# Optimization experiments

Measured on AMD Instinct MI355X. Metric: run time of the kernel, lower is better.

The kernel has to match this reference:

```python
import jax, jax.numpy as jnp
import numpy as np

B, S, V, D, C = 2048, 256, 30522, 768, 100


def setup_inputs() -> dict:
    key = jax.random.key(0)
    k_ids, k_mask, k_emb, k_w1, k_b1, k_w2, k_b2 = jax.random.split(key, 7)
    input_ids = jax.random.randint(k_ids, (B, S), 0, V, dtype=jnp.int64)
    # ensure at least one valid token per row (avoid 0/0 in masked mean)
    attention_mask = jax.random.randint(k_mask, (B, S), 0, 2, dtype=jnp.int64)
    attention_mask = attention_mask.at[:, 0].set(1)
    scale = 1.0 / np.sqrt(D)
    return {
        "input_ids": input_ids,
        "attention_mask": attention_mask,
        "embed_table": jax.random.normal(k_emb, (V, D), dtype=jnp.float32) * 0.02,
        "W1": jax.random.normal(k_w1, (D, D), dtype=jnp.float32) * scale,
        "b1": jax.random.normal(k_b1, (D,), dtype=jnp.float32) * 0.01,
        "W2": jax.random.normal(k_w2, (D, C), dtype=jnp.float32) * scale,
        "b2": jax.random.normal(k_b2, (C,), dtype=jnp.float32) * 0.01,
    }


def reference(input_ids, attention_mask, embed_table, W1, b1, W2, b2):
    # Embedding lookup: [B, S, D]
    word_features = embed_table[input_ids]
    # Fused masked mean pooling over the whole batch (replaces python loop):
    # sum of valid token embeddings / count of valid tokens, per sample.
    mask = attention_mask.astype(word_features.dtype)          # [B, S]
    summed = jnp.einsum("bsd,bs->bd", word_features, mask)     # [B, D]
    counts = jnp.sum(mask, axis=1, keepdims=True)              # [B, 1]
    bow_features = summed / counts                              # [B, D]
    # 2-layer MLP head
    h = jax.nn.relu(bow_features @ W1 + b1)                     # [B, D]
    target_scores = h @ W2 + b2                                 # [B, C]
    return (target_scores, target_scores)
```

## Files before the change

kernel.cpp:

```cpp
#include <hip/hip_runtime.h>

#define B_ 2048
#define S_ 256
#define V_ 30522
#define D_ 768
#define C_ 100
#define NPAD 112

__device__ __forceinline__ unsigned short f2bf(float x) {
  unsigned u = __builtin_bit_cast(unsigned, x);
  u = (u + 0x7fffu + ((u >> 16) & 1u)) >> 16;
  return (unsigned short)u;
}

typedef __attribute__((ext_vector_type(8))) short bf16x8;
typedef __attribute__((ext_vector_type(4))) float f32x4;

__global__ __launch_bounds__(256) void prep_kernel(
    const int* __restrict__ ids, const int* __restrict__ mask,
    const float* __restrict__ w1, const float* __restrict__ w2,
    int* __restrict__ cids, int* __restrict__ cnts,
    unsigned short* __restrict__ w1t, unsigned short* __restrict__ w2t) {
  const int bid = blockIdx.x;
  if (bid < 512) {
    const int wv = threadIdx.x >> 6, lane = threadIdx.x & 63;
    const int b = bid * 4 + wv;
    const int base = b * S_;
    int total = 0;
#pragma unroll
    for (int r = 0; r < S_ / 64; ++r) {
      const int s = r * 64 + lane;
      const int m = mask[base + s];
      const unsigned long long bal = __ballot(m != 0);
      const int pre = __popcll(bal & ((1ull << lane) - 1ull));
      if (m) cids[base + total + pre] = ids[base + s];
      total += __popcll(bal);
    }
    if (lane == 0) cnts[b] = total;
  } else if (bid < 1088) {
    __shared__ float tile[32][33];
    const int local = bid - 512;
    const int k0 = (local % 24) * 32, n0 = (local / 24) * 32;
    const int tx = threadIdx.x & 31, ty = threadIdx.x >> 5;
#pragma unroll
    for (int i = 0; i < 4; ++i)
      tile[ty + i * 8][tx] = w1[(size_t)(k0 + ty + i * 8) * D_ + n0 + tx];
    __syncthreads();
#pragma unroll
    for (int i = 0; i < 4; ++i) {
      const int n = ty + i * 8;
      w1t[(size_t)(n0 + n) * D_ + k0 + tx] = f2bf(tile[tx][n]);
    }
  } else {
    __shared__ float tile[32][33];
    const int local = bid - 1088;
    const int k0 = (local % 24) * 32, n0 = (local / 24) * 32;
    const int tx = threadIdx.x & 31, ty = threadIdx.x >> 5;
#pragma unroll
    for (int i = 0; i < 4; ++i) {
      const int k = k0 + ty + i * 8, n = n0 + tx;
      tile[ty + i * 8][tx] = (n < C_) ? w2[(size_t)k * C_ + n] : 0.f;
    }
    __syncthreads();
#pragma unroll
    for (int i = 0; i < 4; ++i) {
      const int n = n0 + ty + i * 8;
      if (n < NPAD)
        w2t[(size_t)n * D_ + k0 + tx] = f2bf(tile[tx][ty + i * 8]);
    }
  }
}

__global__ __launch_bounds__(256) void pool_sliced(
    const int* __restrict__ cids, const int* __restrict__ cnts,
    const float* __restrict__ table, unsigned short* __restrict__ bowb,
    int pass) {
  __shared__ int sids[4][S_];
  const int bid = blockIdx.x;
  const int chunk = pass * 8 + (bid & 7);
  const int grp = bid >> 3;
  const int wv = threadIdx.x >> 6;
  const int lane = threadIdx.x & 63;
  const int sub = lane >> 3;
  const int cg = lane & 7;
  const int coff = chunk * 32 + cg * 4;

  for (int i = 0; i < 2; ++i) {
    const int smp = grp * 8 + wv * 2 + i;
    const int cnt = cnts[smp];
    const int* cp = cids + (size_t)smp * S_;
#pragma unroll
    for (int r = 0; r < S_ / 64; ++r) {
      const int idx = r * 64 + lane;
      sids[wv][idx] = (idx < cnt) ? cp[idx] : cp[0];
    }
    float a0 = 0.f, a1 = 0.f, a2 = 0.f, a3 = 0.f;
    for (int base = 0; base < cnt; base += 64) {
      float4 v[8];
#pragma unroll
      for (int j = 0; j < 8; ++j) {
        int t = base + j * 8 + sub;
        t = t < S_ ? t : S_ - 1;
        const int id = sids[wv][t];
        v[j] = *reinterpret_cast<const float4*>(table + (size_t)id * D_ + coff);
      }
#pragma unroll
      for (int j = 0; j < 8; ++j) {
        if (base + j * 8 + sub < cnt) {
          a0 += v[j].x; a1 += v[j].y; a2 += v[j].z; a3 += v[j].w;
        }
      }
    }
#pragma unroll
    for (int m = 8; m <= 32; m <<= 1) {
      a0 += __shfl_xor(a0, m);
      a1 += __shfl_xor(a1, m);
      a2 += __shfl_xor(a2, m);
      a3 += __shfl_xor(a3, m);
    }
    if (sub == 0) {
      const float inv = 1.0f / (float)cnt;
      ushort4 o;
      o.x = f2bf(a0 * inv); o.y = f2bf(a1 * inv);
      o.z = f2bf(a2 * inv); o.w = f2bf(a3 * inv);
      *reinterpret_cast<ushort4*>(bowb + (size_t)smp * D_ + coff) = o;
    }
  }
}

#define G1_BM 32
#define G1_BN 64
#define G1_LDK 72

__global__ __launch_bounds__(256) void gemm1_mfma(
    const unsigned short* __restrict__ Ab, const unsigned short* __restrict__ Bt,
    const float* __restrict__ bias, unsigned short* __restrict__ Hb) {
  __shared__ unsigned short As[G1_BM][G1_LDK];
  __shared__ unsigned short Bs[G1_BN][G1_LDK];
  const int tid = threadIdx.x;
  const int bm = blockIdx.x * G1_BM;
  const int bn = blockIdx.y * G1_BN;
  const int w = tid >> 6;
  const int l = tid & 63;
  const int r = l & 15;
  const int g = l >> 4;

  f32x4 acc0 = {0.f, 0.f, 0.f, 0.f};
  f32x4 acc1 = {0.f, 0.f, 0.f, 0.f};

  const int ar = tid >> 3;
  const int kc8 = (tid & 7) * 8;
  const int br = tid >> 3;

  for (int k0 = 0; k0 < D_; k0 += 64) {
    __syncthreads();
    *reinterpret_cast<int4*>(&As[ar][kc8]) =
        *reinterpret_cast<const int4*>(&Ab[(size_t)(bm + ar) * D_ + k0 + kc8]);
    *reinterpret_cast<int4*>(&Bs[br][kc8]) =
        *reinterpret_cast<const int4*>(&Bt[(size_t)(bn + br) * D_ + k0 + kc8]);
    *reinterpret_cast<int4*>(&Bs[br + 32][kc8]) =
        *reinterpret_cast<const int4*>(&Bt[(size_t)(bn + br + 32) * D_ + k0 + kc8]);
    __syncthreads();
    const bf16x8 a00 = *reinterpret_cast<const bf16x8*>(&As[r][g * 8]);
    const bf16x8 a01 = *reinterpret_cast<const bf16x8*>(&As[r][32 + g * 8]);
    const bf16x8 a10 = *reinterpret_cast<const bf16x8*>(&As[16 + r][g * 8]);
    const bf16x8 a11 = *reinterpret_cast<const bf16x8*>(&As[16 + r][32 + g * 8]);
    const bf16x8 b0 = *reinterpret_cast<const bf16x8*>(&Bs[w * 16 + r][g * 8]);
    const bf16x8 b1 = *reinterpret_cast<const bf16x8*>(&Bs[w * 16 + r][32 + g * 8]);
    acc0 = __builtin_amdgcn_mfma_f32_16x16x32_bf16(a00, b0, acc0, 0, 0, 0);
    acc0 = __builtin_amdgcn_mfma_f32_16x16x32_bf16(a01, b1, acc0, 0, 0, 0);
    acc1 = __builtin_amdgcn_mfma_f32_16x16x32_bf16(a10, b0, acc1, 0, 0, 0);
    acc1 = __builtin_amdgcn_mfma_f32_16x16x32_bf16(a11, b1, acc1, 0, 0, 0);
  }

  const int col = bn + w * 16 + r;
  const float bb = bias[col];
#pragma unroll
  for (int q = 0; q < 4; ++q) {
    const int row0 = bm + g * 4 + q;
    float v0 = acc0[q] + bb;
    v0 = v0 > 0.f ? v0 : 0.f;
    Hb[(size_t)row0 * D_ + col] = f2bf(v0);
    float v1 = acc1[q] + bb;
    v1 = v1 > 0.f ? v1 : 0.f;
    Hb[(size_t)(row0 + 16) * D_ + col] = f2bf(v1);
  }
}

__global__ __launch_bounds__(64) void gemm2_mfma(
    const unsigned short* __restrict__ Hb, const unsigned short* __restrict__ w2t,
    const float* __restrict__ b2, float* __restrict__ out) {
  const int bm = blockIdx.x * 16;
  const int bn = blockIdx.y * 16;
  const int l = threadIdx.x;
  const int r = l & 15;
  const int g = l >> 4;

  const unsigned short* ap = Hb + (size_t)(bm + r) * D_ + g * 8;
  const unsigned short* bp = w2t + (size_t)(bn + r) * D_ + g * 8;

  f32x4 acc = {0.f, 0.f, 0.f, 0.f};
#pragma unroll
  for (int k0 = 0; k0 < D_; k0 += 32) {
    const bf16x8 av = *reinterpret_cast<const bf16x8*>(ap + k0);
    const bf16x8 bv = *reinterpret_cast<const bf16x8*>(bp + k0);
    acc = __builtin_amdgcn_mfma_f32_16x16x32_bf16(av, bv, acc, 0, 0, 0);
  }

  const int col = bn + r;
  if (col < C_) {
    const float bb = b2[col];
#pragma unroll
    for (int q = 0; q < 4; ++q) {
      const int row = bm + g * 4 + q;
      const float v = acc[q] + bb;
      out[(size_t)row * C_ + col] = v;
      out[(size_t)row * C_ + col + (size_t)B_ * C_] = v;
    }
  }
}

extern "C" void kernel_launch(void* const* d_in, const int* in_sizes, int n_in,
                              void* d_out, int out_size, void* d_ws,
                              size_t ws_size, hipStream_t stream) {
  const int* ids = (const int*)d_in[0];
  const int* mask = (const int*)d_in[1];
  const float* table = (const float*)d_in[2];
  const float* W1 = (const float*)d_in[3];
  const float* b1 = (const float*)d_in[4];
  const float* W2 = (const float*)d_in[5];
  const float* b2 = (const float*)d_in[6];
  float* out = (float*)d_out;

  const size_t BOWB = (size_t)B_ * D_ * 2;
  const size_t HBB  = (size_t)B_ * D_ * 2;
  const size_t W1TB = (size_t)D_ * D_ * 2;
  const size_t W2TB = (size_t)NPAD * D_ * 2;
  const size_t CIDB = (size_t)B_ * S_ * 4;

  char* p = (char*)d_ws;
  unsigned short* bowb = (unsigned short*)p;
  unsigned short* hb   = (unsigned short*)(p + BOWB);
  unsigned short* w1t  = (unsigned short*)(p + BOWB + HBB);
  unsigned short* w2t  = (unsigned short*)(p + BOWB + HBB + W1TB);
  int* cids            = (int*)(p + BOWB + HBB + W1TB + W2TB);
  int* cnts            = (int*)(p + BOWB + HBB + W1TB + W2TB + CIDB);

  prep_kernel<<<1184, 256, 0, stream>>>(ids, mask, W1, W2, cids, cnts, w1t, w2t);
  pool_sliced<<<2048, 256, 0, stream>>>(cids, cnts, table, bowb, 0);
  pool_sliced<<<2048, 256, 0, stream>>>(cids, cnts, table, bowb, 1);
  pool_sliced<<<2048, 256, 0, stream>>>(cids, cnts, table, bowb, 2);
  gemm1_mfma<<<dim3(B_ / G1_BM, D_ / G1_BN), 256, 0, stream>>>(bowb, w1t, b1, hb);
  gemm2_mfma<<<dim3(B_ / 16, NPAD / 16), 64, 0, stream>>>(hb, w2t, b2, out);
}
```

Baseline: 95.53 us.

## Pin pooling column slices to XCCs via hardware ID and atomic work queue

The pooling kernel now reads the hardware XCC id and uses it to pick which 32-column slice of the embedding table a block handles, so each XCC's L2 only holds its own slice. Blocks take sample groups from a per-slice atomic counter, and the first blocks warm that XCC's L2 by touching a range of table rows. Counters are zeroed in an extra prep block. The aim is fewer L2 misses and less cross-die traffic during the random gathers, at the cost of atomics, extra syncs and a warm-up read.

```diff
diff --git a/kernel.cpp b/kernel.cpp
--- a/kernel.cpp
+++ b/kernel.cpp
@@ -7,6 +7,8 @@
 #define C_ 100
 #define NPAD 112
 
+#define XCC_ID_IMM 6164
+
 __device__ __forceinline__ unsigned short f2bf(float x) {
   unsigned u = __builtin_bit_cast(unsigned, x);
   u = (u + 0x7fffu + ((u >> 16) & 1u)) >> 16;
@@ -20,7 +22,8 @@
     const int* __restrict__ ids, const int* __restrict__ mask,
     const float* __restrict__ w1, const float* __restrict__ w2,
     int* __restrict__ cids, int* __restrict__ cnts,
-    unsigned short* __restrict__ w1t, unsigned short* __restrict__ w2t) {
+    unsigned short* __restrict__ w1t, unsigned short* __restrict__ w2t,
+    int* __restrict__ ctrs) {
   const int bid = blockIdx.x;
   if (bid < 512) {
     const int wv = threadIdx.x >> 6, lane = threadIdx.x & 63;
@@ -51,7 +54,7 @@
       const int n = ty + i * 8;
       w1t[(size_t)(n0 + n) * D_ + k0 + tx] = f2bf(tile[tx][n]);
     }
-  } else {
+  } else if (bid < 1184) {
     __shared__ float tile[32][33];
     const int local = bid - 1088;
     const int k0 = (local % 24) * 32, n0 = (local / 24) * 32;
@@ -68,63 +71,92 @@
       if (n < NPAD)
         w2t[(size_t)n * D_ + k0 + tx] = f2bf(tile[tx][ty + i * 8]);
     }
-  }
-}
+  } else {
+    if (threadIdx.x < 32) ctrs[threadIdx.x] = 0;
+  }
+}
+
+#define NGRP 256
+#define WARM_ROWS 120
 
 __global__ __launch_bounds__(256) void pool_sliced(
     const int* __restrict__ cids, const int* __restrict__ cnts,
     const float* __restrict__ table, unsigned short* __restrict__ bowb,
-    int pass) {
+    int* __restrict__ ctrs, int pass) {
   __shared__ int sids[4][S_];
-  const int bid = blockIdx.x;
-  const int chunk = pass * 8 + (bid & 7);
-  const int grp = bid >> 3;
-  const int wv = threadIdx.x >> 6;
-  const int lane = threadIdx.x & 63;
+  __shared__ int s_grp;
+  const int tid = threadIdx.x;
+  const int xcc = __builtin_amdgcn_s_getreg(XCC_ID_IMM) & 7;
+  const int chunk = pass * 8 + xcc;
+  const int coff0 = chunk * 32;
+
+  const int wv = tid >> 6;
+  const int lane = tid & 63;
   const int sub = lane >> 3;
   const int cg = lane & 7;
-  const int coff = chunk * 32 + cg * 4;
-
-  for (int i = 0; i < 2; ++i) {
-    const int smp = grp * 8 + wv * 2 + i;
-    const int cnt = cnts[smp];
-    const int* cp = cids + (size_t)smp * S_;
-#pragma unroll
-    for (int r = 0; r < S_ / 64; ++r) {
-      const int idx = r * 64 + lane;
-      sids[wv][idx] = (idx < cnt) ? cp[idx] : cp[0];
-    }
-    float a0 = 0.f, a1 = 0.f, a2 = 0.f, a3 = 0.f;
-    for (int base = 0; base < cnt; base += 64) {
-      float4 v[8];
-#pragma unroll
-      for (int j = 0; j < 8; ++j) {
-        int t = base + j * 8 + sub;
-        t = t < S_ ? t : S_ - 1;
-        const int id = sids[wv][t];
-        v[j] = *reinterpret_cast<const float4*>(table + (size_t)id * D_ + coff);
-      }
-#pragma unroll
-      for (int j = 0; j < 8; ++j) {
-        if (base + j * 8 + sub < cnt) {
-          a0 += v[j].x; a1 += v[j].y; a2 += v[j].z; a3 += v[j].w;
+  const int coff = coff0 + cg * 4;
+
+  if (tid == 0) s_grp = atomicAdd(&ctrs[chunk], 1);
+  __syncthreads();
+  int grp = s_grp;
+
+  if (grp < NGRP) {
+    const int r0 = grp * WARM_ROWS;
+    const int nr = (V_ - r0) < WARM_ROWS ? (V_ - r0) : WARM_ROWS;
+    float dummy = 0.f;
+    for (int i = tid; i < nr * 32; i += 256) {
+      const int row = r0 + (i >> 5);
+      dummy += table[(size_t)row * D_ + coff0 + (i & 31)];
+    }
+    asm volatile("" :: "v"(dummy));
+  }
+
+  while (grp < NGRP) {
+    for (int i = 0; i < 2; ++i) {
+      const int smp = grp * 8 + wv * 2 + i;
+      const int cnt = cnts[smp];
+      const int* cp = cids + (size_t)smp * S_;
+#pragma unroll
+      for (int r = 0; r < S_ / 64; ++r) {
+        const int idx = r * 64 + lane;
+        sids[wv][idx] = (idx < cnt) ? cp[idx] : cp[0];
+      }
+      float a0 = 0.f, a1 = 0.f, a2 = 0.f, a3 = 0.f;
+      for (int base = 0; base < cnt; base += 64) {
+        float4 v[8];
+#pragma unroll
+        for (int j = 0; j < 8; ++j) {
+          int t = base + j * 8 + sub;
+          t = t < S_ ? t : S_ - 1;
+          const int id = sids[wv][t];
+          v[j] = *reinterpret_cast<const float4*>(table + (size_t)id * D_ + coff);
         }
-      }
-    }
-#pragma unroll
-    for (int m = 8; m <= 32; m <<= 1) {
-      a0 += __shfl_xor(a0, m);
-      a1 += __shfl_xor(a1, m);
-      a2 += __shfl_xor(a2, m);
-      a3 += __shfl_xor(a3, m);
-    }
-    if (sub == 0) {
-      const float inv = 1.0f / (float)cnt;
-      ushort4 o;
-      o.x = f2bf(a0 * inv); o.y = f2bf(a1 * inv);
-      o.z = f2bf(a2 * inv); o.w = f2bf(a3 * inv);
-      *reinterpret_cast<ushort4*>(bowb + (size_t)smp * D_ + coff) = o;
-    }
+#pragma unroll
+        for (int j = 0; j < 8; ++j) {
+          if (base + j * 8 + sub < cnt) {
+            a0 += v[j].x; a1 += v[j].y; a2 += v[j].z; a3 += v[j].w;
+          }
+        }
+      }
+#pragma unroll
+      for (int m = 8; m <= 32; m <<= 1) {
+        a0 += __shfl_xor(a0, m);
+        a1 += __shfl_xor(a1, m);
+        a2 += __shfl_xor(a2, m);
+        a3 += __shfl_xor(a3, m);
+      }
+      if (sub == 0) {
+        const float inv = 1.0f / (float)cnt;
+        ushort4 o;
+        o.x = f2bf(a0 * inv); o.y = f2bf(a1 * inv);
+        o.z = f2bf(a2 * inv); o.w = f2bf(a3 * inv);
+        *reinterpret_cast<ushort4*>(bowb + (size_t)smp * D_ + coff) = o;
+      }
+    }
+    __syncthreads();
+    if (tid == 0) s_grp = atomicAdd(&ctrs[chunk], 1);
+    __syncthreads();
+    grp = s_grp;
   }
 }
 
@@ -150,16 +182,15 @@
 
   const int ar = tid >> 3;
   const int kc8 = (tid & 7) * 8;
-  const int br = tid >> 3;
 
   for (int k0 = 0; k0 < D_; k0 += 64) {
     __syncthreads();
     *reinterpret_cast<int4*>(&As[ar][kc8]) =
         *reinterpret_cast<const int4*>(&Ab[(size_t)(bm + ar) * D_ + k0 + kc8]);
-    *reinterpret_cast<int4*>(&Bs[br][kc8]) =
-        *reinterpret_cast<const int4*>(&Bt[(size_t)(bn + br) * D_ + k0 + kc8]);
-    *reinterpret_cast<int4*>(&Bs[br + 32][kc8]) =
-        *reinterpret_cast<const int4*>(&Bt[(size_t)(bn + br + 32) * D_ + k0 + kc8]);
+    *reinterpret_cast<int4*>(&Bs[ar][kc8]) =
+        *reinterpret_cast<const int4*>(&Bt[(size_t)(bn + ar) * D_ + k0 + kc8]);
+    *reinterpret_cast<int4*>(&Bs[ar + 32][kc8]) =
+        *reinterpret_cast<const int4*>(&Bt[(size_t)(bn + ar + 32) * D_ + k0 + kc8]);
     __syncthreads();
     const bf16x8 a00 = *reinterpret_cast<const bf16x8*>(&As[r][g * 8]);
     const bf16x8 a01 = *reinterpret_cast<const bf16x8*>(&As[r][32 + g * 8]);
@@ -237,6 +268,7 @@
   const size_t W1TB = (size_t)D_ * D_ * 2;
   const size_t W2TB = (size_t)NPAD * D_ * 2;
   const size_t CIDB = (size_t)B_ * S_ * 4;
+  const size_t CNTB = (size_t)B_ * 4;
 
   char* p = (char*)d_ws;
   unsigned short* bowb = (unsigned short*)p;
@@ -245,11 +277,13 @@
   unsigned short* w2t  = (unsigned short*)(p + BOWB + HBB + W1TB);
   int* cids            = (int*)(p + BOWB + HBB + W1TB + W2TB);
   int* cnts            = (int*)(p + BOWB + HBB + W1TB + W2TB + CIDB);
-
-  prep_kernel<<<1184, 256, 0, stream>>>(ids, mask, W1, W2, cids, cnts, w1t, w2t);
-  pool_sliced<<<2048, 256, 0, stream>>>(cids, cnts, table, bowb, 0);
-  pool_sliced<<<2048, 256, 0, stream>>>(cids, cnts, table, bowb, 1);
-  pool_sliced<<<2048, 256, 0, stream>>>(cids, cnts, table, bowb, 2);
+  int* ctrs            = (int*)(p + BOWB + HBB + W1TB + W2TB + CIDB + CNTB);
+
+  prep_kernel<<<1185, 256, 0, stream>>>(ids, mask, W1, W2, cids, cnts, w1t,
+                                        w2t, ctrs);
+  pool_sliced<<<2048, 256, 0, stream>>>(cids, cnts, table, bowb, ctrs, 0);
+  pool_sliced<<<2048, 256, 0, stream>>>(cids, cnts, table, bowb, ctrs, 1);
+  pool_sliced<<<2048, 256, 0, stream>>>(cids, cnts, table, bowb, ctrs, 2);
   gemm1_mfma<<<dim3(B_ / G1_BM, D_ / G1_BN), 256, 0, stream>>>(bowb, w1t, b1, hb);
   gemm2_mfma<<<dim3(B_ / 16, NPAD / 16), 64, 0, stream>>>(hb, w2t, b2, out);
 }
```

New measurement: 202.5 us. +111.9%, slower.

## Fuse three pooling passes into one kernel and drop per-token masking

Applied to the files above, without the earlier changes.

Merges the three pool_sliced launches into a single launch that loops over the three column passes internally, cutting launch overhead and inter-kernel gaps. The inner accumulation drops the per-token bounds check and clamp: padded slots are filled with the first valid id, summed unconditionally, and then corrected by subtracting the padding count times that row. This shortens the inner loop, but each block now does three times the work serially, and the padding correction can introduce small floating-point differences. The remaining edits rename variables in prep_kernel and gemm1 and do not change behavior.

```diff
diff --git a/kernel.cpp b/kernel.cpp
--- a/kernel.cpp
+++ b/kernel.cpp
@@ -22,8 +22,9 @@
     int* __restrict__ cids, int* __restrict__ cnts,
     unsigned short* __restrict__ w1t, unsigned short* __restrict__ w2t) {
   const int bid = blockIdx.x;
+  const int t = threadIdx.x;
   if (bid < 512) {
-    const int wv = threadIdx.x >> 6, lane = threadIdx.x & 63;
+    const int wv = t >> 6, lane = t & 63;
     const int b = bid * 4 + wv;
     const int base = b * S_;
     int total = 0;
@@ -41,7 +42,7 @@
     __shared__ float tile[32][33];
     const int local = bid - 512;
     const int k0 = (local % 24) * 32, n0 = (local / 24) * 32;
-    const int tx = threadIdx.x & 31, ty = threadIdx.x >> 5;
+    const int tx = t & 31, ty = t >> 5;
 #pragma unroll
     for (int i = 0; i < 4; ++i)
       tile[ty + i * 8][tx] = w1[(size_t)(k0 + ty + i * 8) * D_ + n0 + tx];
@@ -55,7 +56,7 @@
     __shared__ float tile[32][33];
     const int local = bid - 1088;
     const int k0 = (local % 24) * 32, n0 = (local / 24) * 32;
-    const int tx = threadIdx.x & 31, ty = threadIdx.x >> 5;
+    const int tx = t & 31, ty = t >> 5;
 #pragma unroll
     for (int i = 0; i < 4; ++i) {
       const int k = k0 + ty + i * 8, n = n0 + tx;
@@ -73,57 +74,60 @@
 
 __global__ __launch_bounds__(256) void pool_sliced(
     const int* __restrict__ cids, const int* __restrict__ cnts,
-    const float* __restrict__ table, unsigned short* __restrict__ bowb,
-    int pass) {
+    const float* __restrict__ table, unsigned short* __restrict__ bowb) {
   __shared__ int sids[4][S_];
   const int bid = blockIdx.x;
-  const int chunk = pass * 8 + (bid & 7);
   const int grp = bid >> 3;
   const int wv = threadIdx.x >> 6;
   const int lane = threadIdx.x & 63;
   const int sub = lane >> 3;
   const int cg = lane & 7;
-  const int coff = chunk * 32 + cg * 4;
-
-  for (int i = 0; i < 2; ++i) {
-    const int smp = grp * 8 + wv * 2 + i;
-    const int cnt = cnts[smp];
-    const int* cp = cids + (size_t)smp * S_;
-#pragma unroll
-    for (int r = 0; r < S_ / 64; ++r) {
-      const int idx = r * 64 + lane;
-      sids[wv][idx] = (idx < cnt) ? cp[idx] : cp[0];
-    }
-    float a0 = 0.f, a1 = 0.f, a2 = 0.f, a3 = 0.f;
-    for (int base = 0; base < cnt; base += 64) {
-      float4 v[8];
-#pragma unroll
-      for (int j = 0; j < 8; ++j) {
-        int t = base + j * 8 + sub;
-        t = t < S_ ? t : S_ - 1;
-        const int id = sids[wv][t];
-        v[j] = *reinterpret_cast<const float4*>(table + (size_t)id * D_ + coff);
-      }
-#pragma unroll
-      for (int j = 0; j < 8; ++j) {
-        if (base + j * 8 + sub < cnt) {
+
+  for (int pass = 0; pass < 3; ++pass) {
+    const int chunk = pass * 8 + (bid & 7);
+    const int coff = chunk * 32 + cg * 4;
+    for (int i = 0; i < 2; ++i) {
+      const int smp = grp * 8 + wv * 2 + i;
+      const int cnt = cnts[smp];
+      const int* cp = cids + (size_t)smp * S_;
+      const int id0 = cp[0];
+#pragma unroll
+      for (int r = 0; r < S_ / 64; ++r) {
+        const int idx = r * 64 + lane;
+        sids[wv][idx] = (idx < cnt) ? cp[idx] : id0;
+      }
+      float a0 = 0.f, a1 = 0.f, a2 = 0.f, a3 = 0.f;
+      const int nb = (cnt + 63) >> 6;
+      for (int b = 0; b < nb; ++b) {
+        float4 v[8];
+#pragma unroll
+        for (int j = 0; j < 8; ++j) {
+          const int id = sids[wv][b * 64 + j * 8 + sub];
+          v[j] = *reinterpret_cast<const float4*>(table + (size_t)id * D_ + coff);
+        }
+#pragma unroll
+        for (int j = 0; j < 8; ++j) {
           a0 += v[j].x; a1 += v[j].y; a2 += v[j].z; a3 += v[j].w;
         }
       }
-    }
-#pragma unroll
-    for (int m = 8; m <= 32; m <<= 1) {
-      a0 += __shfl_xor(a0, m);
-      a1 += __shfl_xor(a1, m);
-      a2 += __shfl_xor(a2, m);
-      a3 += __shfl_xor(a3, m);
-    }
-    if (sub == 0) {
-      const float inv = 1.0f / (float)cnt;
-      ushort4 o;
-      o.x = f2bf(a0 * inv); o.y = f2bf(a1 * inv);
-      o.z = f2bf(a2 * inv); o.w = f2bf(a3 * inv);
-      *reinterpret_cast<ushort4*>(bowb + (size_t)smp * D_ + coff) = o;
+#pragma unroll
+      for (int m = 8; m <= 32; m <<= 1) {
+        a0 += __shfl_xor(a0, m);
+        a1 += __shfl_xor(a1, m);
+        a2 += __shfl_xor(a2, m);
+        a3 += __shfl_xor(a3, m);
+      }
+      if (sub == 0) {
+        const float fp = (float)(nb * 64 - cnt);
+        const float4 v0 =
+            *reinterpret_cast<const float4*>(table + (size_t)id0 * D_ + coff);
+        a0 -= fp * v0.x; a1 -= fp * v0.y; a2 -= fp * v0.z; a3 -= fp * v0.w;
+        const float inv = 1.0f / (float)cnt;
+        ushort4 o;
+        o.x = f2bf(a0 * inv); o.y = f2bf(a1 * inv);
+        o.z = f2bf(a2 * inv); o.w = f2bf(a3 * inv);
+        *reinterpret_cast<ushort4*>(bowb + (size_t)smp * D_ + coff) = o;
+      }
     }
   }
 }
@@ -150,16 +154,15 @@
 
   const int ar = tid >> 3;
   const int kc8 = (tid & 7) * 8;
-  const int br = tid >> 3;
 
   for (int k0 = 0; k0 < D_; k0 += 64) {
     __syncthreads();
     *reinterpret_cast<int4*>(&As[ar][kc8]) =
         *reinterpret_cast<const int4*>(&Ab[(size_t)(bm + ar) * D_ + k0 + kc8]);
-    *reinterpret_cast<int4*>(&Bs[br][kc8]) =
-        *reinterpret_cast<const int4*>(&Bt[(size_t)(bn + br) * D_ + k0 + kc8]);
-    *reinterpret_cast<int4*>(&Bs[br + 32][kc8]) =
-        *reinterpret_cast<const int4*>(&Bt[(size_t)(bn + br + 32) * D_ + k0 + kc8]);
+    *reinterpret_cast<int4*>(&Bs[ar][kc8]) =
+        *reinterpret_cast<const int4*>(&Bt[(size_t)(bn + ar) * D_ + k0 + kc8]);
+    *reinterpret_cast<int4*>(&Bs[ar + 32][kc8]) =
+        *reinterpret_cast<const int4*>(&Bt[(size_t)(bn + ar + 32) * D_ + k0 + kc8]);
     __syncthreads();
     const bf16x8 a00 = *reinterpret_cast<const bf16x8*>(&As[r][g * 8]);
     const bf16x8 a01 = *reinterpret_cast<const bf16x8*>(&As[r][32 + g * 8]);
@@ -247,9 +250,7 @@
   int* cnts            = (int*)(p + BOWB + HBB + W1TB + W2TB + CIDB);
 
   prep_kernel<<<1184, 256, 0, stream>>>(ids, mask, W1, W2, cids, cnts, w1t, w2t);
-  pool_sliced<<<2048, 256, 0, stream>>>(cids, cnts, table, bowb, 0);
-  pool_sliced<<<2048, 256, 0, stream>>>(cids, cnts, table, bowb, 1);
-  pool_sliced<<<2048, 256, 0, stream>>>(cids, cnts, table, bowb, 2);
+  pool_sliced<<<2048, 256, 0, stream>>>(cids, cnts, table, bowb);
   gemm1_mfma<<<dim3(B_ / G1_BM, D_ / G1_BN), 256, 0, stream>>>(bowb, w1t, b1, hb);
   gemm2_mfma<<<dim3(B_ / 16, NPAD / 16), 64, 0, stream>>>(hb, w2t, b2, out);
 }
```

Measured after the change: 97.56 us. 1.02x slower.
